# Kernel optimization log

Measured on AMD Instinct MI355X. Metric: run time of the kernel, lower is better.

Reference implementation:

```python
import jax, jax.numpy as jnp
import numpy as np

BS, N, D_IN, HID, D_OUT = 16, 256, 128, 128, 128


def setup_inputs() -> dict:
    key = jax.random.key(0)
    ks = jax.random.split(key, 10)
    s = 0.02
    return {
        "x": jax.random.normal(ks[0], (BS, N, D_IN), dtype=jnp.float32),
        "adj": jax.random.randint(ks[1], (BS, N, N), 0, 2, dtype=jnp.int32),
        "W_fc": jax.random.normal(ks[2], (D_IN, HID), dtype=jnp.float32) * s,
        "b_fc": jnp.zeros((HID,), dtype=jnp.float32),
        "W_a1": jax.random.normal(ks[3], (2 * HID, HID), dtype=jnp.float32) * s,
        "b_a1": jnp.zeros((HID,), dtype=jnp.float32),
        "w_a2": jax.random.normal(ks[4], (HID,), dtype=jnp.float32) * s,
        "b_a2": jnp.zeros((), dtype=jnp.float32),
        "W_out": jax.random.normal(ks[5], (HID, D_OUT), dtype=jnp.float32) * s,
        "b_out": jnp.zeros((D_OUT,), dtype=jnp.float32),
    }


def reference(x, adj, W_fc, b_fc, W_a1, b_a1, w_a2, b_a2, W_out, b_out):
    # h = fc(x): (bs, n, hid)
    h = jnp.einsum("bnd,dh->bnh", x, W_fc) + b_fc
    # attn first layer on concat([h_i, h_j]) decomposes into two half-projections
    # (same math as Linear(2*hid, hid) on the concatenated pair features).
    a_i = jnp.einsum("bnh,hk->bnk", h, W_a1[:HID])  # contribution of h_i
    a_j = jnp.einsum("bnh,hk->bnk", h, W_a1[HID:])  # contribution of h_j
    pre = a_i[:, :, None, :] + a_j[:, None, :, :] + b_a1  # (bs, n, n, hid)
    e = jnp.einsum("bijk,k->bij", jax.nn.relu(pre), w_a2) + b_a2  # (bs, n, n)
    e = jnp.where(adj == 0, jnp.float32(-1e9), e)
    attn = jax.nn.softmax(e, axis=-1)
    h_prime = jnp.einsum("bij,bjh->bih", attn, h)
    out = jnp.einsum("bih,ho->bio", h_prime, W_out) + b_out
    return out
```

## Files before the change

kernel.cpp:

```cpp
#include <hip/hip_runtime.h>

#define BS  16
#define NN  256
#define HID 128

__device__ __forceinline__ int xcd_swz(int bid) {
    return (bid & 7) * 64 + (bid >> 3);
}

__global__ __launch_bounds__(512, 4) void gat_k1(
    const float* __restrict__ x, const float* __restrict__ W_fc,
    const float* __restrict__ b_fc, const float* __restrict__ W_a1,
    const float* __restrict__ b_a1,
    float* __restrict__ aiT, float* __restrict__ ajT, float* __restrict__ h)
{
    __shared__ __align__(16) float xs[8][HID];
    __shared__ __align__(16) float hs[8][HID];
    __shared__ __align__(16) float red[4][2][8][HID];

    const int tid = threadIdx.x;
    const int k   = tid & 127;
    const int q   = tid >> 7;
    const int swz = xcd_swz(blockIdx.x);
    const int r0  = swz * 8;
    const int b   = r0 >> 8;
    const int n0  = r0 & 255;

    for (int t = tid; t < 8 * HID; t += 512)
        xs[t >> 7][t & 127] = x[r0 * HID + t];
    __syncthreads();

    {
        float acc[8] = {0,0,0,0,0,0,0,0};
        const int dq = 32 * q;
        #pragma unroll 2
        for (int d = 0; d < 32; d += 4) {
            float w[4];
            #pragma unroll
            for (int t = 0; t < 4; ++t) w[t] = W_fc[(dq + d + t) * HID + k];
            #pragma unroll
            for (int r = 0; r < 8; ++r) {
                const float4 xv = *(const float4*)&xs[r][dq + d];
                acc[r] += xv.x * w[0] + xv.y * w[1] + xv.z * w[2] + xv.w * w[3];
            }
        }
        #pragma unroll
        for (int r = 0; r < 8; ++r) red[q][0][r][k] = acc[r];
    }
    __syncthreads();

    {
        const float bf = b_fc[k];
        #pragma unroll
        for (int r2 = 0; r2 < 2; ++r2) {
            const int r = 2 * q + r2;
            const float hv = (red[0][0][r][k] + red[1][0][r][k])
                           + (red[2][0][r][k] + red[3][0][r][k]) + bf;
            hs[r][k] = hv;
            h[(r0 + r) * HID + k] = hv;
        }
    }
    __syncthreads();

    {
        float ai_a[8] = {0,0,0,0,0,0,0,0};
        float aj_a[8] = {0,0,0,0,0,0,0,0};
        const int dq = 32 * q;
        #pragma unroll 2
        for (int d = 0; d < 32; d += 4) {
            float wi[4], wj[4];
            #pragma unroll
            for (int t = 0; t < 4; ++t) {
                wi[t] = W_a1[(dq + d + t) * HID + k];
                wj[t] = W_a1[(HID + dq + d + t) * HID + k];
            }
            #pragma unroll
            for (int r = 0; r < 8; ++r) {
                const float4 hv = *(const float4*)&hs[r][dq + d];
                ai_a[r] += hv.x * wi[0] + hv.y * wi[1] + hv.z * wi[2] + hv.w * wi[3];
                aj_a[r] += hv.x * wj[0] + hv.y * wj[1] + hv.z * wj[2] + hv.w * wj[3];
            }
        }
        #pragma unroll
        for (int r = 0; r < 8; ++r) {
            red[q][0][r][k] = ai_a[r];
            red[q][1][r][k] = aj_a[r];
        }
    }
    __syncthreads();

    {
        const int is_aj = q >> 1;
        const int rb4   = (q & 1) * 4;
        const float bias = is_aj ? 0.f : b_a1[k];
        float4 v;
        v.x = (red[0][is_aj][rb4 + 0][k] + red[1][is_aj][rb4 + 0][k])
            + (red[2][is_aj][rb4 + 0][k] + red[3][is_aj][rb4 + 0][k]) + bias;
        v.y = (red[0][is_aj][rb4 + 1][k] + red[1][is_aj][rb4 + 1][k])
            + (red[2][is_aj][rb4 + 1][k] + red[3][is_aj][rb4 + 1][k]) + bias;
        v.z = (red[0][is_aj][rb4 + 2][k] + red[1][is_aj][rb4 + 2][k])
            + (red[2][is_aj][rb4 + 2][k] + red[3][is_aj][rb4 + 2][k]) + bias;
        v.w = (red[0][is_aj][rb4 + 3][k] + red[1][is_aj][rb4 + 3][k])
            + (red[2][is_aj][rb4 + 3][k] + red[3][is_aj][rb4 + 3][k]) + bias;
        float* dst = (is_aj ? ajT : aiT) + (b * HID + k) * NN + n0 + rb4;
        *(float4*)dst = v;
    }
}

__global__ __launch_bounds__(512, 4) void gat_k2(
    const float* __restrict__ aiT, const float* __restrict__ ajT,
    const float* __restrict__ h,  const int* __restrict__ adj,
    const float* __restrict__ w_a2, const float* __restrict__ b_a2,
    const float* __restrict__ W_out, const float* __restrict__ b_out,
    float* __restrict__ out)
{
    __shared__ __align__(16) float4 aiwp[HID][4];
    __shared__ __align__(16) float  buf[2][8][NN];
    __shared__ __align__(16) float  ep[8][NN];

    const int tid = threadIdx.x;
    const int swz = xcd_swz(blockIdx.x);
    const int b   = swz >> 5;
    const int i0  = (swz & 31) * 8;
    const int wv  = tid >> 6, lane = tid & 63;

    {
        const int kk = tid >> 2, rp2 = tid & 3;
        const float* ar = aiT + (b * HID + kk) * NN + i0 + 2 * rp2;
        float4 v;
        v.x = ar[0];
        v.y = ar[1];
        v.z = w_a2[kk];
        v.w = 0.f;
        aiwp[kk][rp2] = v;
    }

    const int4 am = *(const int4*)(adj + (b * NN + i0 + wv) * NN + 4 * lane);
    __syncthreads();

    const int kh = wv >> 2, rp = wv & 3;
    {
        const float* ajp = ajT + (b * HID + kh * 64) * NN + 4 * lane;
        float4 acc0 = {0,0,0,0}, acc1 = {0,0,0,0}, saw = {0,0,0,0};
        const int kb = kh * 64;
        #pragma unroll 8
        for (int t = 0; t < 64; ++t) {
            const float4 a4 = *(const float4*)(ajp + t * NN);
            const float4 aw = aiwp[kb + t][rp];
            saw.x  = __builtin_fmaf(a4.x, aw.z, saw.x);
            saw.y  = __builtin_fmaf(a4.y, aw.z, saw.y);
            saw.z  = __builtin_fmaf(a4.z, aw.z, saw.z);
            saw.w  = __builtin_fmaf(a4.w, aw.z, saw.w);
            acc0.x = __builtin_fmaf(fmaxf(aw.x, -a4.x), aw.z, acc0.x);
            acc0.y = __builtin_fmaf(fmaxf(aw.x, -a4.y), aw.z, acc0.y);
            acc0.z = __builtin_fmaf(fmaxf(aw.x, -a4.z), aw.z, acc0.z);
            acc0.w = __builtin_fmaf(fmaxf(aw.x, -a4.w), aw.z, acc0.w);
            acc1.x = __builtin_fmaf(fmaxf(aw.y, -a4.x), aw.z, acc1.x);
            acc1.y = __builtin_fmaf(fmaxf(aw.y, -a4.y), aw.z, acc1.y);
            acc1.z = __builtin_fmaf(fmaxf(aw.y, -a4.z), aw.z, acc1.z);
            acc1.w = __builtin_fmaf(fmaxf(aw.y, -a4.w), aw.z, acc1.w);
        }
        const float4 e0 = {acc0.x + saw.x, acc0.y + saw.y,
                           acc0.z + saw.z, acc0.w + saw.w};
        const float4 e1 = {acc1.x + saw.x, acc1.y + saw.y,
                           acc1.z + saw.z, acc1.w + saw.w};
        *(float4*)&buf[kh][2 * rp + 0][4 * lane] = e0;
        *(float4*)&buf[kh][2 * rp + 1][4 * lane] = e1;
    }
    __syncthreads();

    {
        const float ba2 = b_a2[0];
        const float4 u = *(const float4*)&buf[0][wv][4 * lane];
        const float4 v = *(const float4*)&buf[1][wv][4 * lane];
        const float e0 = am.x ? u.x + v.x + ba2 : -1e9f;
        const float e1 = am.y ? u.y + v.y + ba2 : -1e9f;
        const float e2 = am.z ? u.z + v.z + ba2 : -1e9f;
        const float e3 = am.w ? u.w + v.w + ba2 : -1e9f;
        float m = fmaxf(fmaxf(e0, e1), fmaxf(e2, e3));
        #pragma unroll
        for (int off = 32; off; off >>= 1) m = fmaxf(m, __shfl_xor(m, off));
        const float p0 = __expf(e0 - m), p1 = __expf(e1 - m);
        const float p2 = __expf(e2 - m), p3 = __expf(e3 - m);
        float s = (p0 + p1) + (p2 + p3);
        #pragma unroll
        for (int off = 32; off; off >>= 1) s += __shfl_xor(s, off);
        const float inv = 1.f / s;
        const float4 pv = {p0 * inv, p1 * inv, p2 * inv, p3 * inv};
        *(float4*)&ep[wv][4 * lane] = pv;
    }
    __syncthreads();

    float* red = &buf[0][0][0];
    const int qh = wv & 3, rh = wv >> 2;
    {
        float2 o[4];
        #pragma unroll
        for (int r = 0; r < 4; ++r) { o[r].x = 0.f; o[r].y = 0.f; }
        const int jb = qh * 64;
        const float* hb = h + (b * NN + jb) * HID + 2 * lane;
        #pragma unroll 2
        for (int jq = 0; jq < 64; jq += 4) {
            const float2 h0 = *(const float2*)(hb + (jq + 0) * HID);
            const float2 h1 = *(const float2*)(hb + (jq + 1) * HID);
            const float2 h2 = *(const float2*)(hb + (jq + 2) * HID);
            const float2 h3 = *(const float2*)(hb + (jq + 3) * HID);
            #pragma unroll
            for (int r = 0; r < 4; ++r) {
                const float4 pv = *(const float4*)&ep[rh * 4 + r][jb + jq];
                o[r].x += pv.x * h0.x + pv.y * h1.x + pv.z * h2.x + pv.w * h3.x;
                o[r].y += pv.x * h0.y + pv.y * h1.y + pv.z * h2.y + pv.w * h3.y;
            }
        }
        #pragma unroll
        for (int r = 0; r < 4; ++r)
            *(float2*)&red[(qh * 8 + rh * 4 + r) * HID + 2 * lane] = o[r];
    }
    __syncthreads();

    float* hp = (float*)&aiwp[0][0];
    {
        const int k = tid & 127, qh2 = tid >> 7;
        #pragma unroll
        for (int r2 = 0; r2 < 2; ++r2) {
            const int r = 2 * qh2 + r2;
            hp[r * HID + k] =
                (red[(0 + r) * HID + k]  + red[(8 + r) * HID + k]) +
                (red[(16 + r) * HID + k] + red[(24 + r) * HID + k]);
        }
    }
    __syncthreads();

    {
        const int k = tid & 127, q4 = tid >> 7;
        const float bo = b_out[k];
        float o0 = bo, o1 = bo;
        #pragma unroll 2
        for (int d0 = 0; d0 < HID; d0 += 4) {
            float w[4];
            #pragma unroll
            for (int t = 0; t < 4; ++t) w[t] = W_out[(d0 + t) * HID + k];
            const float4 hA = *(const float4*)&hp[(2 * q4 + 0) * HID + d0];
            const float4 hB = *(const float4*)&hp[(2 * q4 + 1) * HID + d0];
            o0 += hA.x * w[0] + hA.y * w[1] + hA.z * w[2] + hA.w * w[3];
            o1 += hB.x * w[0] + hB.y * w[1] + hB.z * w[2] + hB.w * w[3];
        }
        out[(b * NN + i0 + 2 * q4 + 0) * HID + k] = o0;
        out[(b * NN + i0 + 2 * q4 + 1) * HID + k] = o1;
    }
}

extern "C" void kernel_launch(void* const* d_in, const int* in_sizes, int n_in,
                              void* d_out, int out_size, void* d_ws, size_t ws_size,
                              hipStream_t stream) {
    const float* x     = (const float*)d_in[0];
    const int*   adj   = (const int*)  d_in[1];
    const float* W_fc  = (const float*)d_in[2];
    const float* b_fc  = (const float*)d_in[3];
    const float* W_a1  = (const float*)d_in[4];
    const float* b_a1  = (const float*)d_in[5];
    const float* w_a2  = (const float*)d_in[6];
    const float* b_a2  = (const float*)d_in[7];
    const float* W_out = (const float*)d_in[8];
    const float* b_out = (const float*)d_in[9];
    float* out = (float*)d_out;

    float* ws  = (float*)d_ws;
    float* aiT = ws;
    float* ajT = ws + BS * NN * HID;
    float* hbuf= ws + 2 * BS * NN * HID;

    gat_k1<<<BS * NN / 8, 512, 0, stream>>>(x, W_fc, b_fc, W_a1, b_a1,
                                            aiT, ajT, hbuf);
    gat_k2<<<BS * (NN / 8), 512, 0, stream>>>(aiT, ajT, hbuf, adj, w_a2, b_a2,
                                              W_out, b_out, out);
}
```

Measured before the change: 42.50 us.

## Give each wave one full query row in GAT attention kernel

Restructures gat_k2 so each of the 8 waves owns one query row end to end: it scores all 128 hidden channels for its row, runs the softmax, and computes the attention-weighted sum over all 256 neighbors itself. This drops the cross-wave split of the hidden dimension and neighbor range, along with the partial-sum buffers, their LDS reductions and several __syncthreads barriers. In exchange, each wave reads the full ajT and h slices for the batch once per row instead of sharing the loads across row pairs, which raises global/L2 traffic per block. The old fmax(a,-b)+saw trick is also replaced by a plain relu(a+b)*w form.

```diff
diff --git a/kernel.cpp b/kernel.cpp
--- a/kernel.cpp
+++ b/kernel.cpp
@@ -114,69 +114,47 @@
     const float* __restrict__ W_out, const float* __restrict__ b_out,
     float* __restrict__ out)
 {
-    __shared__ __align__(16) float4 aiwp[HID][4];
-    __shared__ __align__(16) float  buf[2][8][NN];
-    __shared__ __align__(16) float  ep[8][NN];
+    __shared__ __align__(16) float2 aiw[8][HID];
+    __shared__ __align__(16) float  pscr[8][NN];
+    __shared__ __align__(16) float  hp[8][HID];
 
     const int tid = threadIdx.x;
     const int swz = xcd_swz(blockIdx.x);
     const int b   = swz >> 5;
     const int i0  = (swz & 31) * 8;
-    const int wv  = tid >> 6, lane = tid & 63;
-
-    {
-        const int kk = tid >> 2, rp2 = tid & 3;
-        const float* ar = aiT + (b * HID + kk) * NN + i0 + 2 * rp2;
-        float4 v;
-        v.x = ar[0];
-        v.y = ar[1];
-        v.z = w_a2[kk];
-        v.w = 0.f;
-        aiwp[kk][rp2] = v;
-    }
-
-    const int4 am = *(const int4*)(adj + (b * NN + i0 + wv) * NN + 4 * lane);
-    __syncthreads();
-
-    const int kh = wv >> 2, rp = wv & 3;
-    {
-        const float* ajp = ajT + (b * HID + kh * 64) * NN + 4 * lane;
-        float4 acc0 = {0,0,0,0}, acc1 = {0,0,0,0}, saw = {0,0,0,0};
-        const int kb = kh * 64;
+    const int w   = tid >> 6, lane = tid & 63;
+    const int r   = i0 + w;
+
+    #pragma unroll
+    for (int t = 0; t < 2; ++t) {
+        const int kk = t * 64 + lane;
+        float2 v;
+        v.x = aiT[(b * HID + kk) * NN + r];
+        v.y = w_a2[kk];
+        aiw[w][kk] = v;
+    }
+    const int4 am = *(const int4*)(adj + (b * NN + r) * NN + 4 * lane);
+
+    float4 acc = {0.f, 0.f, 0.f, 0.f};
+    {
+        const float* ajp = ajT + b * HID * NN + 4 * lane;
         #pragma unroll 8
-        for (int t = 0; t < 64; ++t) {
-            const float4 a4 = *(const float4*)(ajp + t * NN);
-            const float4 aw = aiwp[kb + t][rp];
-            saw.x  = __builtin_fmaf(a4.x, aw.z, saw.x);
-            saw.y  = __builtin_fmaf(a4.y, aw.z, saw.y);
-            saw.z  = __builtin_fmaf(a4.z, aw.z, saw.z);
-            saw.w  = __builtin_fmaf(a4.w, aw.z, saw.w);
-            acc0.x = __builtin_fmaf(fmaxf(aw.x, -a4.x), aw.z, acc0.x);
-            acc0.y = __builtin_fmaf(fmaxf(aw.x, -a4.y), aw.z, acc0.y);
-            acc0.z = __builtin_fmaf(fmaxf(aw.x, -a4.z), aw.z, acc0.z);
-            acc0.w = __builtin_fmaf(fmaxf(aw.x, -a4.w), aw.z, acc0.w);
-            acc1.x = __builtin_fmaf(fmaxf(aw.y, -a4.x), aw.z, acc1.x);
-            acc1.y = __builtin_fmaf(fmaxf(aw.y, -a4.y), aw.z, acc1.y);
-            acc1.z = __builtin_fmaf(fmaxf(aw.y, -a4.z), aw.z, acc1.z);
-            acc1.w = __builtin_fmaf(fmaxf(aw.y, -a4.w), aw.z, acc1.w);
-        }
-        const float4 e0 = {acc0.x + saw.x, acc0.y + saw.y,
-                           acc0.z + saw.z, acc0.w + saw.w};
-        const float4 e1 = {acc1.x + saw.x, acc1.y + saw.y,
-                           acc1.z + saw.z, acc1.w + saw.w};
-        *(float4*)&buf[kh][2 * rp + 0][4 * lane] = e0;
-        *(float4*)&buf[kh][2 * rp + 1][4 * lane] = e1;
-    }
-    __syncthreads();
+        for (int kk = 0; kk < HID; ++kk) {
+            const float4 a4 = *(const float4*)(ajp + kk * NN);
+            const float2 aw = aiw[w][kk];
+            acc.x = __builtin_fmaf(fmaxf(aw.x + a4.x, 0.f), aw.y, acc.x);
+            acc.y = __builtin_fmaf(fmaxf(aw.x + a4.y, 0.f), aw.y, acc.y);
+            acc.z = __builtin_fmaf(fmaxf(aw.x + a4.z, 0.f), aw.y, acc.z);
+            acc.w = __builtin_fmaf(fmaxf(aw.x + a4.w, 0.f), aw.y, acc.w);
+        }
+    }
 
     {
         const float ba2 = b_a2[0];
-        const float4 u = *(const float4*)&buf[0][wv][4 * lane];
-        const float4 v = *(const float4*)&buf[1][wv][4 * lane];
-        const float e0 = am.x ? u.x + v.x + ba2 : -1e9f;
-        const float e1 = am.y ? u.y + v.y + ba2 : -1e9f;
-        const float e2 = am.z ? u.z + v.z + ba2 : -1e9f;
-        const float e3 = am.w ? u.w + v.w + ba2 : -1e9f;
+        const float e0 = am.x ? acc.x + ba2 : -1e9f;
+        const float e1 = am.y ? acc.y + ba2 : -1e9f;
+        const float e2 = am.z ? acc.z + ba2 : -1e9f;
+        const float e3 = am.w ? acc.w + ba2 : -1e9f;
         float m = fmaxf(fmaxf(e0, e1), fmaxf(e2, e3));
         #pragma unroll
         for (int off = 32; off; off >>= 1) m = fmaxf(m, __shfl_xor(m, off));
@@ -187,66 +165,39 @@
         for (int off = 32; off; off >>= 1) s += __shfl_xor(s, off);
         const float inv = 1.f / s;
         const float4 pv = {p0 * inv, p1 * inv, p2 * inv, p3 * inv};
-        *(float4*)&ep[wv][4 * lane] = pv;
-    }
-    __syncthreads();
-
-    float* red = &buf[0][0][0];
-    const int qh = wv & 3, rh = wv >> 2;
-    {
-        float2 o[4];
-        #pragma unroll
-        for (int r = 0; r < 4; ++r) { o[r].x = 0.f; o[r].y = 0.f; }
-        const int jb = qh * 64;
-        const float* hb = h + (b * NN + jb) * HID + 2 * lane;
-        #pragma unroll 2
-        for (int jq = 0; jq < 64; jq += 4) {
-            const float2 h0 = *(const float2*)(hb + (jq + 0) * HID);
-            const float2 h1 = *(const float2*)(hb + (jq + 1) * HID);
-            const float2 h2 = *(const float2*)(hb + (jq + 2) * HID);
-            const float2 h3 = *(const float2*)(hb + (jq + 3) * HID);
-            #pragma unroll
-            for (int r = 0; r < 4; ++r) {
-                const float4 pv = *(const float4*)&ep[rh * 4 + r][jb + jq];
-                o[r].x += pv.x * h0.x + pv.y * h1.x + pv.z * h2.x + pv.w * h3.x;
-                o[r].y += pv.x * h0.y + pv.y * h1.y + pv.z * h2.y + pv.w * h3.y;
-            }
-        }
-        #pragma unroll
-        for (int r = 0; r < 4; ++r)
-            *(float2*)&red[(qh * 8 + rh * 4 + r) * HID + 2 * lane] = o[r];
-    }
-    __syncthreads();
-
-    float* hp = (float*)&aiwp[0][0];
-    {
-        const int k = tid & 127, qh2 = tid >> 7;
-        #pragma unroll
-        for (int r2 = 0; r2 < 2; ++r2) {
-            const int r = 2 * qh2 + r2;
-            hp[r * HID + k] =
-                (red[(0 + r) * HID + k]  + red[(8 + r) * HID + k]) +
-                (red[(16 + r) * HID + k] + red[(24 + r) * HID + k]);
-        }
-    }
-    __syncthreads();
-
-    {
-        const int k = tid & 127, q4 = tid >> 7;
+        *(float4*)&pscr[w][4 * lane] = pv;
+    }
+
+    {
+        float2 o = {0.f, 0.f};
+        const float* hb = h + b * NN * HID + 2 * lane;
+        #pragma unroll 4
+        for (int j = 0; j < NN; ++j) {
+            const float2 hv = *(const float2*)(hb + j * HID);
+            const float pj = pscr[w][j];
+            o.x = __builtin_fmaf(pj, hv.x, o.x);
+            o.y = __builtin_fmaf(pj, hv.y, o.y);
+        }
+        *(float2*)&hp[w][2 * lane] = o;
+    }
+    __syncthreads();
+
+    {
+        const int k = tid & 127, q = tid >> 7;
         const float bo = b_out[k];
         float o0 = bo, o1 = bo;
         #pragma unroll 2
         for (int d0 = 0; d0 < HID; d0 += 4) {
-            float w[4];
-            #pragma unroll
-            for (int t = 0; t < 4; ++t) w[t] = W_out[(d0 + t) * HID + k];
-            const float4 hA = *(const float4*)&hp[(2 * q4 + 0) * HID + d0];
-            const float4 hB = *(const float4*)&hp[(2 * q4 + 1) * HID + d0];
-            o0 += hA.x * w[0] + hA.y * w[1] + hA.z * w[2] + hA.w * w[3];
-            o1 += hB.x * w[0] + hB.y * w[1] + hB.z * w[2] + hB.w * w[3];
-        }
-        out[(b * NN + i0 + 2 * q4 + 0) * HID + k] = o0;
-        out[(b * NN + i0 + 2 * q4 + 1) * HID + k] = o1;
+            float wv[4];
+            #pragma unroll
+            for (int t = 0; t < 4; ++t) wv[t] = W_out[(d0 + t) * HID + k];
+            const float4 hA = *(const float4*)&hp[2 * q + 0][d0];
+            const float4 hB = *(const float4*)&hp[2 * q + 1][d0];
+            o0 += hA.x * wv[0] + hA.y * wv[1] + hA.z * wv[2] + hA.w * wv[3];
+            o1 += hB.x * wv[0] + hB.y * wv[1] + hB.z * wv[2] + hB.w * wv[3];
+        }
+        out[(b * NN + i0 + 2 * q + 0) * HID + k] = o0;
+        out[(b * NN + i0 + 2 * q + 1) * HID + k] = o1;
     }
 }
 
```

Measured after the change: 68.05 us. +60.1%, slower.
